# Optimization experiments

Hardware: AMD Instinct MI355X
Metric: run time of the kernel (lower is better)

Reference implementation:

```python
import jax, jax.numpy as jnp
import numpy as np

L, B, S, CACHE = 2, 1, 2048, 2048
H, HKV, D, DM, FF, V = 16, 8, 128, 2048, 8192, 32000
EPS = 1e-6
ROPE_BASE = 10000.0


def setup_inputs() -> dict:
    key = jax.random.key(0)
    ks = jax.random.split(key, 18)
    std = 0.02
    r = lambda k, shape: (jax.random.normal(k, shape, dtype=jnp.float32) * std)
    return {
        "input_ids": jax.random.randint(ks[0], (B, S), 0, V),
        "embed": r(ks[1], (V, DM)),
        "Wq": r(ks[2], (L, DM, H * D)),
        "Wk": r(ks[3], (L, DM, HKV * D)),
        "Wv": r(ks[4], (L, DM, HKV * D)),
        "Wo": r(ks[5], (L, H * D, DM)),
        "Wg": r(ks[6], (L, DM, FF)),
        "Wu": r(ks[7], (L, DM, FF)),
        "Wd": r(ks[8], (L, FF, DM)),
        "ln1": jnp.ones((L, DM), jnp.float32),
        "ln2": jnp.ones((L, DM), jnp.float32),
        "final_norm": jnp.ones((DM,), jnp.float32),
        "lm_head": r(ks[9], (DM, V)),
        "k_cache": jax.random.normal(ks[10], (L, B, H, CACHE, D), jnp.float32),
        "v_cache": jax.random.normal(ks[11], (L, B, H, CACHE, D), jnp.float32),
    }


def rms_norm(x, w):
    return x * jax.lax.rsqrt(jnp.mean(x * x, axis=-1, keepdims=True) + EPS) * w


def apply_rope(x, pos):
    # x: [B,H,T,D], pos: [T]
    inv_freq = 1.0 / (ROPE_BASE ** (jnp.arange(0, D, 2, dtype=jnp.float32) / D))
    f = pos[:, None].astype(jnp.float32) * inv_freq[None, :]  # [T, D/2]
    emb = jnp.concatenate([f, f], axis=-1)                    # [T, D]
    cos, sin = jnp.cos(emb), jnp.sin(emb)
    rot = jnp.concatenate([-x[..., D // 2:], x[..., : D // 2]], axis=-1)
    return x * cos + rot * sin


def decoder_forward(input_ids, embed, Wq, Wk, Wv, Wo, Wg, Wu, Wd,
                    ln1, ln2, final_norm, lm_head, k_cache, v_cache):
    h = embed[input_ids]  # [B,S,DM]
    T = CACHE + S
    q_pos = jnp.arange(CACHE, CACHE + S)
    k_pos = jnp.arange(T)
    # causal mask: query i (global pos CACHE+i) attends keys <= CACHE+i
    mask = k_pos[None, :] <= (CACHE + jnp.arange(S))[:, None]  # [S,T]
    scale = 1.0 / np.sqrt(D)

    def layer(h, params):
        wq, wk, wv, wo, wg, wu, wd, l1, l2, kc, vc = params
        x = rms_norm(h, l1)
        q = (x @ wq).reshape(B, S, H, D).transpose(0, 2, 1, 3)     # [B,H,S,D]
        k = (x @ wk).reshape(B, S, HKV, D).transpose(0, 2, 1, 3)   # [B,HKV,S,D]
        v = (x @ wv).reshape(B, S, HKV, D).transpose(0, 2, 1, 3)
        k = jnp.repeat(k, H // HKV, axis=1)                        # repeat_kv
        v = jnp.repeat(v, H // HKV, axis=1)
        k = jnp.concatenate([kc, k], axis=2)                       # [B,H,T,D]
        v = jnp.concatenate([vc, v], axis=2)
        q = apply_rope(q, q_pos)
        k = apply_rope(k, k_pos)
        scores = jnp.einsum('bhqd,bhkd->bhqk', q, k) * scale
        scores = jnp.where(mask, scores, jnp.float32(-1e30))
        attn = jax.nn.softmax(scores, axis=-1)
        o = jnp.einsum('bhqk,bhkd->bhqd', attn, v)
        o = o.transpose(0, 2, 1, 3).reshape(B, S, H * D) @ wo
        h = h + o
        x = rms_norm(h, l2)
        h = h + (jax.nn.silu(x @ wg) * (x @ wu)) @ wd
        return h, None

    h, _ = jax.lax.scan(layer, h, (Wq, Wk, Wv, Wo, Wg, Wu, Wd, ln1, ln2, k_cache, v_cache))
    h = rms_norm(h, final_norm)
    return (h @ lm_head).astype(jnp.float32)  # logits [B,S,V]


def reference(input_ids, embed, Wq, Wk, Wv, Wo, Wg, Wu, Wd,
              ln1, ln2, final_norm, lm_head, k_cache, v_cache):
    return decoder_forward(input_ids, embed, Wq, Wk, Wv, Wo, Wg, Wu, Wd,
                           ln1, ln2, final_norm, lm_head, k_cache, v_cache)
```

## Files before the change

### kernel.cpp

```cpp
#include <hip/hip_runtime.h>

typedef __attribute__((ext_vector_type(8))) short bfrag8;
typedef __attribute__((ext_vector_type(4))) short bfrag4;
typedef __attribute__((ext_vector_type(4))) float facc4;

#define DEV_INLINE __device__ __forceinline__

DEV_INLINE short f2bf(float f) {
    union { float f; unsigned u; } x; x.f = f;
    unsigned r = (x.u + 0x7FFFu + ((x.u >> 16) & 1u)) >> 16;
    return (short)r;
}

DEV_INLINE float bf2f(short s) {
    union { unsigned u; float f; } x;
    x.u = ((unsigned)(unsigned short)s) << 16;
    return x.f;
}

DEV_INLINE unsigned pack_bf2(float a, float b) {
    return (unsigned)(unsigned short)f2bf(a) | ((unsigned)(unsigned short)f2bf(b) << 16);
}

#define GL2LDS(gp, lp) __builtin_amdgcn_global_load_lds( \
    (const __attribute__((address_space(1))) void*)(gp), \
    (__attribute__((address_space(3))) void*)(lp), 16, 0, 0)

#define MFMA16(a, b, c) __builtin_amdgcn_mfma_f32_16x16x32_bf16((a), (b), (c), 0, 0, 0)

__global__ __launch_bounds__(256) void embed_kernel(const int* __restrict__ ids,
                                                    const float* __restrict__ emb,
                                                    float* __restrict__ h) {
    int s = blockIdx.x;
    int id = ids[s];
    const float* src = emb + (size_t)id * 2048;
    float* dst = h + (size_t)s * 2048;
    int t = threadIdx.x;
    float4 a = *(const float4*)(src + t * 8);
    float4 b = *(const float4*)(src + t * 8 + 4);
    *(float4*)(dst + t * 8) = a;
    *(float4*)(dst + t * 8 + 4) = b;
}

__global__ __launch_bounds__(256) void rmsnorm_bf16_kernel(const float* __restrict__ in,
                                                           const float* __restrict__ w,
                                                           short* __restrict__ out) {
    int row = blockIdx.x;
    const float* x = in + (size_t)row * 2048;
    short* y = out + (size_t)row * 2048;
    int t = threadIdx.x;
    float4 a = *(const float4*)(x + t * 8);
    float4 b = *(const float4*)(x + t * 8 + 4);
    float ss = a.x*a.x + a.y*a.y + a.z*a.z + a.w*a.w
             + b.x*b.x + b.y*b.y + b.z*b.z + b.w*b.w;
#pragma unroll
    for (int off = 32; off >= 1; off >>= 1) ss += __shfl_xor(ss, off);
    __shared__ float red[4];
    if ((t & 63) == 0) red[t >> 6] = ss;
    __syncthreads();
    float tot = red[0] + red[1] + red[2] + red[3];
    float sc = rsqrtf(tot * (1.0f / 2048.0f) + 1e-6f);
    float4 wa = *(const float4*)(w + t * 8);
    float4 wb = *(const float4*)(w + t * 8 + 4);
    bfrag8 o;
    o[0] = f2bf(a.x * sc * wa.x); o[1] = f2bf(a.y * sc * wa.y);
    o[2] = f2bf(a.z * sc * wa.z); o[3] = f2bf(a.w * sc * wa.w);
    o[4] = f2bf(b.x * sc * wb.x); o[5] = f2bf(b.y * sc * wb.y);
    o[6] = f2bf(b.z * sc * wb.z); o[7] = f2bf(b.w * sc * wb.w);
    *(bfrag8*)(y + t * 8) = o;
}

__global__ __launch_bounds__(256) void wconv_kernel(const float* __restrict__ W,
                                                    short* __restrict__ Wt,
                                                    int K, int N) {
    __shared__ short Lt[64][72];
    int k0 = blockIdx.x * 64, n0 = blockIdx.y * 64;
    int tid = threadIdx.x;
    int r = tid >> 4, c = (tid & 15) * 4;
#pragma unroll
    for (int j = 0; j < 4; ++j) {
        int k = r + j * 16;
        float4 v = *(const float4*)(W + (size_t)(k0 + k) * N + n0 + c);
        Lt[c + 0][k] = f2bf(v.x); Lt[c + 1][k] = f2bf(v.y);
        Lt[c + 2][k] = f2bf(v.z); Lt[c + 3][k] = f2bf(v.w);
    }
    __syncthreads();
    int n = tid >> 3, kk = (tid & 7) * 8;
#pragma unroll
    for (int j = 0; j < 2; ++j)
        *(bfrag8*)(Wt + (size_t)(n0 + n + j * 32) * K + k0 + kk) = *(const bfrag8*)&Lt[n + j * 32][kk];
}

template<int OUT>
__global__ __launch_bounds__(256, 2) void gemmR(const short* __restrict__ A,
                                                const short* __restrict__ Bt,
                                                float* __restrict__ C,
                                                int K, int N) {
    constexpr int ASLOT = 128 * 64;
    constexpr int BOFF = 4 * ASLOT;
    __shared__ short lds[4 * 256 * 32];
    char* ldsb = (char*)lds;
    int tid = threadIdx.x;
    int lane = tid & 63, wave = tid >> 6;
    int wm = wave >> 1, wn = wave & 1;
    int lr = lane & 15, lg = lane >> 4;

    int gx = gridDim.x;
    int nwg = gx * gridDim.y;
    int b = blockIdx.y * gx + blockIdx.x;
    int q8 = nwg >> 3, r8 = nwg & 7;
    int xcd = b & 7, idx = b >> 3;
    int lb = (xcd < r8) ? (xcd * (q8 + 1) + idx) : (r8 * (q8 + 1) + (xcd - r8) * q8 + idx);
    int bm = (lb % gx) * 128, bn = (lb / gx) * 128;

    facc4 acc[4][4];
#pragma unroll
    for (int m = 0; m < 4; ++m)
#pragma unroll
        for (int n = 0; n < 4; ++n) acc[m][n] = (facc4){0.f, 0.f, 0.f, 0.f};

    int rs = tid >> 2;
    int cs = (tid & 3) ^ ((rs >> 1) & 3);
    const size_t sK = (size_t)K;
    const short* Ag0 = A + (size_t)(bm + rs) * sK + cs * 8;
    const short* Ag1 = A + (size_t)(bm + rs + 64) * sK + cs * 8;
    const short* Bg0 = Bt + (size_t)(bn + rs) * sK + cs * 8;
    const short* Bg1 = Bt + (size_t)(bn + rs + 64) * sK + cs * 8;

    auto stage = [&](int u) {
        int sl = u & 3;
        int ko = u * 32;
        char* Ad = ldsb + sl * ASLOT + tid * 16;
        char* Bd = ldsb + BOFF + sl * ASLOT + tid * 16;
        GL2LDS(Ag0 + ko, Ad);
        GL2LDS(Ag1 + ko, Ad + 4096);
        GL2LDS(Bg0 + ko, Bd);
        GL2LDS(Bg1 + ko, Bd + 4096);
    };

    int NT = K >> 5;
    stage(0); stage(1); stage(2);

    int arow[4], brow[4];
#pragma unroll
    for (int m = 0; m < 4; ++m) arow[m] = wm * 64 + m * 16 + lr;
#pragma unroll
    for (int n = 0; n < 4; ++n) brow[n] = wn * 64 + n * 16 + lr;

    for (int t = 0; t < NT; ++t) {
        if (t < NT - 2)       asm volatile("s_waitcnt vmcnt(8)" ::: "memory");
        else if (t == NT - 2) asm volatile("s_waitcnt vmcnt(4)" ::: "memory");
        else                  asm volatile("s_waitcnt vmcnt(0)" ::: "memory");
        __builtin_amdgcn_s_barrier();
        __builtin_amdgcn_sched_barrier(0);
        const char* Ab = ldsb + (t & 3) * ASLOT;
        const char* Bb = ldsb + BOFF + (t & 3) * ASLOT;
        bfrag8 af[4], bf[4];
#pragma unroll
        for (int m = 0; m < 4; ++m) {
            int r = arow[m];
            af[m] = *(const bfrag8*)(Ab + r * 64 + ((lg ^ ((r >> 1) & 3)) << 4));
        }
#pragma unroll
        for (int n = 0; n < 4; ++n) {
            int r = brow[n];
            bf[n] = *(const bfrag8*)(Bb + r * 64 + ((lg ^ ((r >> 1) & 3)) << 4));
        }
        if (t + 3 < NT) stage(t + 3);
        __builtin_amdgcn_s_setprio(1);
#pragma unroll
        for (int m = 0; m < 4; ++m)
#pragma unroll
            for (int n = 0; n < 4; ++n)
                acc[m][n] = MFMA16(af[m], bf[n], acc[m][n]);
        __builtin_amdgcn_s_setprio(0);
    }

    int crow = bm + wm * 64 + lg * 4;
    int ccol = bn + wn * 64 + lr;
#pragma unroll
    for (int m = 0; m < 4; ++m)
#pragma unroll
        for (int n = 0; n < 4; ++n)
#pragma unroll
            for (int r = 0; r < 4; ++r) {
                size_t ci = (size_t)(crow + m * 16 + r) * N + ccol + n * 16;
                if constexpr (OUT == 0)      C[ci] = acc[m][n][r];
                else if constexpr (OUT == 1) C[ci] = C[ci] + acc[m][n][r];
                else                         ((short*)C)[ci] = f2bf(acc[m][n][r]);
            }
}

template<int OUT>
__global__ __launch_bounds__(512, 2) void gemm8p(const short* __restrict__ A,
                                                 const short* __restrict__ Bt,
                                                 float* __restrict__ C,
                                                 int K, int N) {
    __shared__ short lds[49152];
    char* ldsb = (char*)lds;
    int tid = threadIdx.x;
    int lane = tid & 63, wave = tid >> 6;
    int wm = wave >> 2, wn = wave & 3;
    int lr = lane & 15, lg = lane >> 4;

    int gx = gridDim.x;
    int nwg = gx * gridDim.y;
    int b = blockIdx.y * gx + blockIdx.x;
    int q8 = nwg >> 3, r8 = nwg & 7;
    int xcd = b & 7, idx = b >> 3;
    int lb = (xcd < r8) ? (xcd * (q8 + 1) + idx) : (r8 * (q8 + 1) + (xcd - r8) * q8 + idx);
    int bm = (lb % gx) * 256, bn = (lb / gx) * 256;

    facc4 acc[8][4];
#pragma unroll
    for (int m = 0; m < 8; ++m)
#pragma unroll
        for (int n = 0; n < 4; ++n) acc[m][n] = (facc4){0.f, 0.f, 0.f, 0.f};

    int rs = tid >> 2;
    int cs = (tid & 3) ^ ((rs >> 1) & 3);
    const size_t sK = (size_t)K;
    const short* Agl = A + (size_t)(bm + rs) * sK + cs * 8;
    const short* Agh = A + (size_t)(bm + rs + 128) * sK + cs * 8;
    const short* Bgl = Bt + (size_t)(bn + rs) * sK + cs * 8;
    const short* Bgh = Bt + (size_t)(bn + rs + 128) * sK + cs * 8;

    auto stage = [&](int h) {
        int sb = (h % 3) * 16384;
        int ko = h * 32;
        GL2LDS(Agl + ko, ldsb + sb + tid * 16);
        GL2LDS(Agh + ko, ldsb + sb + 8192 + tid * 16);
        GL2LDS(Bgl + ko, ldsb + 49152 + sb + tid * 16);
        GL2LDS(Bgh + ko, ldsb + 49152 + sb + 8192 + tid * 16);
    };

    int H = K >> 5;
    stage(0); stage(1);

    int arow[8], brow[4];
#pragma unroll
    for (int m = 0; m < 8; ++m) arow[m] = wm * 128 + m * 16 + lr;
#pragma unroll
    for (int n = 0; n < 4; ++n) brow[n] = wn * 64 + n * 16 + lr;

    for (int h = 0; h < H; ++h) {
        if (h + 1 < H) asm volatile("s_waitcnt vmcnt(4)" ::: "memory");
        else           asm volatile("s_waitcnt vmcnt(0)" ::: "memory");
        __builtin_amdgcn_s_barrier();
        __builtin_amdgcn_sched_barrier(0);
        const char* Ah = ldsb + (h % 3) * 16384;
        const char* Bh = ldsb + 49152 + (h % 3) * 16384;
        bfrag8 af[8], bf[4];
#pragma unroll
        for (int m = 0; m < 8; ++m) {
            int r = arow[m];
            af[m] = *(const bfrag8*)(Ah + r * 64 + ((lg ^ ((r >> 1) & 3)) << 4));
        }
#pragma unroll
        for (int n = 0; n < 2; ++n) {
            int r = brow[n];
            bf[n] = *(const bfrag8*)(Bh + r * 64 + ((lg ^ ((r >> 1) & 3)) << 4));
        }
        if (h + 2 < H) stage(h + 2);
        __builtin_amdgcn_s_barrier();
        asm volatile("s_waitcnt lgkmcnt(0)" ::: "memory");
        __builtin_amdgcn_sched_barrier(0);
        __builtin_amdgcn_s_setprio(1);
#pragma unroll
        for (int m = 0; m < 8; ++m) {
            acc[m][0] = MFMA16(af[m], bf[0], acc[m][0]);
            acc[m][1] = MFMA16(af[m], bf[1], acc[m][1]);
        }
        __builtin_amdgcn_s_setprio(0);
        __builtin_amdgcn_s_barrier();
#pragma unroll
        for (int n = 2; n < 4; ++n) {
            int r = brow[n];
            bf[n] = *(const bfrag8*)(Bh + r * 64 + ((lg ^ ((r >> 1) & 3)) << 4));
        }
        __builtin_amdgcn_s_barrier();
        asm volatile("s_waitcnt lgkmcnt(0)" ::: "memory");
        __builtin_amdgcn_sched_barrier(0);
        __builtin_amdgcn_s_setprio(1);
#pragma unroll
        for (int m = 0; m < 8; ++m) {
            acc[m][2] = MFMA16(af[m], bf[2], acc[m][2]);
            acc[m][3] = MFMA16(af[m], bf[3], acc[m][3]);
        }
        __builtin_amdgcn_s_setprio(0);
    }

    int crow = bm + wm * 128 + lg * 4;
    int ccol = bn + wn * 64 + lr;
#pragma unroll
    for (int m = 0; m < 8; ++m)
#pragma unroll
        for (int n = 0; n < 4; ++n)
#pragma unroll
            for (int r = 0; r < 4; ++r) {
                size_t ci = (size_t)(crow + m * 16 + r) * N + ccol + n * 16;
                if constexpr (OUT == 0)      C[ci] = acc[m][n][r];
                else if constexpr (OUT == 1) C[ci] = C[ci] + acc[m][n][r];
                else                         ((short*)C)[ci] = f2bf(acc[m][n][r]);
            }
}

#define ROPE_C 0.20762050593046010f
#define INV2PI 0.15915494309189535f
#define TWOPI  6.283185307179586f
#define QK_SCALE 0.08838834764831845f

DEV_INLINE void rope_sc(float pos, int j, float* s, float* c) {
    float f = pos * exp2f(-(float)j * ROPE_C);
    float r = f * INV2PI;
    r -= floorf(r);
    __sincosf(r * TWOPI, s, c);
}

__global__ __launch_bounds__(128) void prep_q_kernel(const float* __restrict__ qkv,
                                                     short* __restrict__ Qb) {
    int h = blockIdx.x, s = blockIdx.y, d = threadIdx.x;
    const float* src = qkv + (size_t)s * 4096 + h * 128;
    float x = src[d], xp = src[d ^ 64];
    float sn, c;
    rope_sc((float)(2048 + s), d & 63, &sn, &c);
    float o = (d < 64) ? (x * c - xp * sn) : (x * c + xp * sn);
    Qb[((size_t)h * 2048 + s) * 128 + d] = f2bf(o * QK_SCALE);
}

__global__ __launch_bounds__(128) void prep_k_kernel(const float* __restrict__ kc,
                                                     const float* __restrict__ qkv,
                                                     short* __restrict__ Kf) {
    int h = blockIdx.x, t = blockIdx.y, d = threadIdx.x;
    float x, xp;
    if (t < 2048) {
        const float* src = kc + ((size_t)h * 2048 + t) * 128;
        x = src[d]; xp = src[d ^ 64];
    } else {
        const float* src = qkv + (size_t)(t - 2048) * 4096 + 2048 + (h >> 1) * 128;
        x = src[d]; xp = src[d ^ 64];
    }
    float sn, c;
    rope_sc((float)t, d & 63, &sn, &c);
    float o = (d < 64) ? (x * c - xp * sn) : (x * c + xp * sn);
    Kf[((size_t)h * 4096 + t) * 128 + d] = f2bf(o);
}

__global__ __launch_bounds__(256) void prep_v_kernel(const float* __restrict__ vc,
                                                     const float* __restrict__ qkv,
                                                     short* __restrict__ Vt) {
    int h = blockIdx.x;
    int t0 = blockIdx.y * 64;
    __shared__ short Lt[128][72];
    int tid = threadIdx.x;
    int r = tid >> 2;
    int c0 = (tid & 3) * 32;
    int t = t0 + r;
    const float* src = (t < 2048)
        ? vc + ((size_t)h * 2048 + t) * 128 + c0
        : qkv + (size_t)(t - 2048) * 4096 + 3072 + (h >> 1) * 128 + c0;
#pragma unroll
    for (int i = 0; i < 32; i += 4) {
        float4 v = *(const float4*)(src + i);
        Lt[c0 + i + 0][r] = f2bf(v.x);
        Lt[c0 + i + 1][r] = f2bf(v.y);
        Lt[c0 + i + 2][r] = f2bf(v.z);
        Lt[c0 + i + 3][r] = f2bf(v.w);
    }
    __syncthreads();
    int d = tid >> 1;
    int hh = (tid & 1) * 32;
    short* dst = Vt + ((size_t)h * 128 + d) * 4096 + t0 + hh;
    const short* srcl = &Lt[d][hh];
#pragma unroll
    for (int i = 0; i < 32; i += 8)
        *(bfrag8*)(dst + i) = *(const bfrag8*)(srcl + i);
}

__global__ __launch_bounds__(256, 4) void attn_kernel(const short* __restrict__ Q,
                                                      const short* __restrict__ Kf,
                                                      const short* __restrict__ Vt,
                                                      float* __restrict__ Op,
                                                      float* __restrict__ Ml,
                                                      float* __restrict__ Ll) {
    int h = blockIdx.x;
    int qb = blockIdx.y * 64;
    int z = blockIdx.z;
    int tid = threadIdx.x;
    int lane = tid & 63, wave = tid >> 6;
    int lr = lane & 15, lg = lane >> 4;
    int qrow = qb + wave * 16;
    int qg = 2048 + qrow + lr;

    __shared__ short Ks[2][4096];
    __shared__ short Vs[2][4096];
    __shared__ short P[4][16][40];

    const short* kbase = Kf + (size_t)h * 4096 * 128;
    const short* vbase = Vt + (size_t)h * 128 * 4096;

    bfrag8 aq[4];
    {
        const short* qp = Q + ((size_t)h * 2048 + qrow + lr) * 128 + lg * 8;
#pragma unroll
        for (int dt = 0; dt < 4; ++dt) aq[dt] = *(const bfrag8*)(qp + dt * 32);
    }
    facc4 o[8];
#pragma unroll
    for (int n = 0; n < 8; ++n) o[n] = (facc4){0.f, 0.f, 0.f, 0.f};
    float m = -1e30f, l = 0.f;

    auto stage = [&](int buf, int t0) {
#pragma unroll
        for (int half = 0; half < 2; ++half) {
            int rk = half * 16 + wave * 4 + (lane >> 4);
            int ck = (lane & 15) ^ (rk & 7);
            GL2LDS(kbase + (size_t)(t0 + rk) * 128 + ck * 8,
                   &Ks[buf][half * 2048 + wave * 512 + lane * 8]);
            int rv = half * 64 + wave * 16 + (lane >> 2);
            int cv = (lane & 3) ^ ((rv >> 1) & 3);
            GL2LDS(vbase + (size_t)rv * 4096 + t0 + cv * 8,
                   &Vs[buf][half * 2048 + wave * 512 + lane * 8]);
        }
    };

    auto process = [&](int buf, int t0) {
        facc4 s0 = (facc4){0.f, 0.f, 0.f, 0.f}, s1 = (facc4){0.f, 0.f, 0.f, 0.f};
        int r0 = lr, r1 = 16 + lr;
#pragma unroll
        for (int dt = 0; dt < 4; ++dt) {
            bfrag8 k0 = *(const bfrag8*)&Ks[buf][r0 * 128 + (((dt * 4 + lg) ^ (r0 & 7)) * 8)];
            bfrag8 k1 = *(const bfrag8*)&Ks[buf][r1 * 128 + (((dt * 4 + lg) ^ (r1 & 7)) * 8)];
            s0 = MFMA16(k0, aq[dt], s0);
            s1 = MFMA16(k1, aq[dt], s1);
        }
        float mx = m;
#pragma unroll
        for (int r = 0; r < 4; ++r) {
            int k0i = t0 + lg * 4 + r;
            if (k0i > qg)      s0[r] = -1e30f;
            if (k0i + 16 > qg) s1[r] = -1e30f;
            mx = fmaxf(mx, fmaxf(s0[r], s1[r]));
        }
        mx = fmaxf(mx, __shfl_xor(mx, 16));
        mx = fmaxf(mx, __shfl_xor(mx, 32));
        if (__any(mx > m + 8.f)) {
            float alpha = __expf(m - mx);
            m = mx;
            l *= alpha;
            float ab[4];
#pragma unroll
            for (int r = 0; r < 4; ++r) ab[r] = __shfl(alpha, lg * 4 + r);
#pragma unroll
            for (int n = 0; n < 8; ++n) {
                o[n][0] *= ab[0]; o[n][1] *= ab[1]; o[n][2] *= ab[2]; o[n][3] *= ab[3];
            }
        }
        float ps = 0.f;
#pragma unroll
        for (int r = 0; r < 4; ++r) {
            s0[r] = __expf(s0[r] - m); ps += s0[r];
            s1[r] = __expf(s1[r] - m); ps += s1[r];
        }
        ps += __shfl_xor(ps, 16);
        ps += __shfl_xor(ps, 32);
        l += ps;
        unsigned* prow = (unsigned*)&P[wave][lr][0];
        prow[lg * 2]     = pack_bf2(s0[0], s0[1]);
        prow[lg * 2 + 1] = pack_bf2(s0[2], s0[3]);
        prow[8 + lg * 2]     = pack_bf2(s1[0], s1[1]);
        prow[8 + lg * 2 + 1] = pack_bf2(s1[2], s1[3]);
        bfrag8 ap = *(const bfrag8*)&P[wave][lr][lg * 8];
#pragma unroll
        for (int n = 0; n < 8; ++n) {
            int rv = n * 16 + lr;
            bfrag8 vf = *(const bfrag8*)&Vs[buf][rv * 32 + ((lg ^ ((rv >> 1) & 3)) * 8)];
            o[n] = MFMA16(ap, vf, o[n]);
        }
    };

    int NT = ((2048 + qb + 63) >> 5) + 1;
    int i0 = z ? (NT >> 1) : 0;
    int i1 = z ? NT : (NT >> 1);

    stage(0, i0 * 32);
    __syncthreads();
    int buf = 0;
    for (int i = i0; i < i1; ++i) {
        if (i + 1 < i1) stage(buf ^ 1, (i + 1) * 32);
        process(buf, i * 32);
        __syncthreads();
        buf ^= 1;
    }

#pragma unroll
    for (int n = 0; n < 8; ++n)
#pragma unroll
        for (int r = 0; r < 4; ++r)
            Op[(size_t)(z * 2048 + qrow + lg * 4 + r) * 2048 + h * 128 + n * 16 + lr] = o[n][r];
    if (lg == 0) {
        Ml[((size_t)z * 16 + h) * 2048 + qrow + lr] = m;
        Ll[((size_t)z * 16 + h) * 2048 + qrow + lr] = l;
    }
}

__global__ __launch_bounds__(256) void attn_combine(const float* __restrict__ Op,
                                                    const float* __restrict__ Ml,
                                                    const float* __restrict__ Ll,
                                                    short* __restrict__ Ob) {
    int row = blockIdx.x, t = threadIdx.x;
    int col0 = t * 8;
    int h = col0 >> 7;
    float m0 = Ml[(size_t)h * 2048 + row], m1 = Ml[(size_t)(16 + h) * 2048 + row];
    float l0 = Ll[(size_t)h * 2048 + row], l1 = Ll[(size_t)(16 + h) * 2048 + row];
    float mm = fmaxf(m0, m1);
    float a0 = __expf(m0 - mm), a1 = __expf(m1 - mm);
    float inv = 1.f / (l0 * a0 + l1 * a1);
    a0 *= inv; a1 *= inv;
    const float* p0 = Op + (size_t)row * 2048 + col0;
    const float* p1 = Op + (size_t)(2048 + row) * 2048 + col0;
    float4 x0 = *(const float4*)p0, x1 = *(const float4*)(p0 + 4);
    float4 y0 = *(const float4*)p1, y1 = *(const float4*)(p1 + 4);
    bfrag8 ov;
    ov[0] = f2bf(x0.x * a0 + y0.x * a1); ov[1] = f2bf(x0.y * a0 + y0.y * a1);
    ov[2] = f2bf(x0.z * a0 + y0.z * a1); ov[3] = f2bf(x0.w * a0 + y0.w * a1);
    ov[4] = f2bf(x1.x * a0 + y1.x * a1); ov[5] = f2bf(x1.y * a0 + y1.y * a1);
    ov[6] = f2bf(x1.z * a0 + y1.z * a1); ov[7] = f2bf(x1.w * a0 + y1.w * a1);
    *(bfrag8*)(Ob + (size_t)row * 2048 + col0) = ov;
}

__global__ __launch_bounds__(256) void silu_fused_kernel(const short* __restrict__ f,
                                                         short* __restrict__ out) {
    size_t v = (size_t)blockIdx.x * 256 + threadIdx.x;
    int r = (int)(v >> 10);
    int c = (int)(v & 1023) * 8;
    bfrag8 g = *(const bfrag8*)(f + (size_t)r * 16384 + c);
    bfrag8 u = *(const bfrag8*)(f + (size_t)r * 16384 + 8192 + c);
    bfrag8 o;
#pragma unroll
    for (int j = 0; j < 8; ++j) {
        float gf = bf2f(g[j]), uf = bf2f(u[j]);
        o[j] = f2bf(gf / (1.f + __expf(-gf)) * uf);
    }
    *(bfrag8*)(out + v * 8) = o;
}

extern "C" void kernel_launch(void* const* d_in, const int* in_sizes, int n_in,
                              void* d_out, int out_size, void* d_ws, size_t ws_size,
                              hipStream_t stream) {
    const int*   ids   = (const int*)d_in[0];
    const float* emb   = (const float*)d_in[1];
    const float* Wq    = (const float*)d_in[2];
    const float* Wk    = (const float*)d_in[3];
    const float* Wv    = (const float*)d_in[4];
    const float* Wo    = (const float*)d_in[5];
    const float* Wg    = (const float*)d_in[6];
    const float* Wu    = (const float*)d_in[7];
    const float* Wd    = (const float*)d_in[8];
    const float* ln1   = (const float*)d_in[9];
    const float* ln2   = (const float*)d_in[10];
    const float* fnorm = (const float*)d_in[11];
    const float* lmh   = (const float*)d_in[12];
    const float* kc    = (const float*)d_in[13];
    const float* vc    = (const float*)d_in[14];
    float* logits = (float*)d_out;

    char* ws = (char*)d_ws;
    float* hbuf   = (float*)(ws + ((size_t)0 << 20));
    short* xb     = (short*)(ws + ((size_t)16 << 20));
    float* qkvbuf = (float*)(ws + ((size_t)24 << 20));
    short* Ob     = (short*)(ws + ((size_t)56 << 20));
    short* wt     = (short*)(ws + ((size_t)64 << 20));
    short* Qb     = (short*)(ws + ((size_t)128 << 20));
    short* Kf     = (short*)(ws + ((size_t)136 << 20));
    short* Vt     = (short*)(ws + ((size_t)152 << 20));
    short* fbuf   = (short*)(ws + ((size_t)168 << 20));
    short* gb     = (short*)(ws + ((size_t)232 << 20));
    float* mlb    = (float*)(ws + ((size_t)264 << 20));
    float* Mlp    = mlb;
    float* Llp    = mlb + 2 * 16 * 2048;
    short* lmwt   = (short*)(ws + ((size_t)64 << 20));

    embed_kernel<<<2048, 256, 0, stream>>>(ids, emb, hbuf);

    for (int l = 0; l < 2; ++l) {
        const float* wq  = Wq + (size_t)l * 2048 * 2048;
        const float* wk  = Wk + (size_t)l * 2048 * 1024;
        const float* wv  = Wv + (size_t)l * 2048 * 1024;
        const float* wo  = Wo + (size_t)l * 2048 * 2048;
        const float* wg  = Wg + (size_t)l * 2048 * 8192;
        const float* wu  = Wu + (size_t)l * 2048 * 8192;
        const float* wd  = Wd + (size_t)l * 8192 * 2048;
        const float* l1  = ln1 + (size_t)l * 2048;
        const float* l2  = ln2 + (size_t)l * 2048;
        const float* kcl = kc + (size_t)l * 16 * 2048 * 128;
        const float* vcl = vc + (size_t)l * 16 * 2048 * 128;

        rmsnorm_bf16_kernel<<<2048, 256, 0, stream>>>(hbuf, l1, xb);
        wconv_kernel<<<dim3(32, 32), 256, 0, stream>>>(wq, wt, 2048, 2048);
        wconv_kernel<<<dim3(32, 16), 256, 0, stream>>>(wk, wt + (size_t)2048 * 2048, 2048, 1024);
        wconv_kernel<<<dim3(32, 16), 256, 0, stream>>>(wv, wt + (size_t)3072 * 2048, 2048, 1024);
        gemmR<0><<<dim3(16, 32), 256, 0, stream>>>(xb, wt, qkvbuf, 2048, 4096);
        prep_q_kernel<<<dim3(16, 2048), 128, 0, stream>>>(qkvbuf, Qb);
        prep_k_kernel<<<dim3(16, 4096), 128, 0, stream>>>(kcl, qkvbuf, Kf);
        prep_v_kernel<<<dim3(16, 64), 256, 0, stream>>>(vcl, qkvbuf, Vt);
        attn_kernel<<<dim3(16, 32, 2), 256, 0, stream>>>(Qb, Kf, Vt, qkvbuf, Mlp, Llp);
        attn_combine<<<2048, 256, 0, stream>>>(qkvbuf, Mlp, Llp, Ob);
        wconv_kernel<<<dim3(32, 32), 256, 0, stream>>>(wo, wt, 2048, 2048);
        gemmR<1><<<dim3(16, 16), 256, 0, stream>>>(Ob, wt, hbuf, 2048, 2048);
        rmsnorm_bf16_kernel<<<2048, 256, 0, stream>>>(hbuf, l2, xb);
        wconv_kernel<<<dim3(32, 128), 256, 0, stream>>>(wg, wt, 2048, 8192);
        wconv_kernel<<<dim3(32, 128), 256, 0, stream>>>(wu, wt + (size_t)8192 * 2048, 2048, 8192);
        gemm8p<2><<<dim3(8, 64), 512, 0, stream>>>(xb, wt, (float*)fbuf, 2048, 16384);
        silu_fused_kernel<<<8192, 256, 0, stream>>>(fbuf, gb);
        wconv_kernel<<<dim3(128, 32), 256, 0, stream>>>(wd, wt, 8192, 2048);
        gemmR<1><<<dim3(16, 16), 256, 0, stream>>>(gb, wt, hbuf, 8192, 2048);
    }
    rmsnorm_bf16_kernel<<<2048, 256, 0, stream>>>(hbuf, fnorm, xb);
    wconv_kernel<<<dim3(32, 500), 256, 0, stream>>>(lmh, lmwt, 2048, 32000);
    gemm8p<0><<<dim3(8, 125), 512, 0, stream>>>(xb, lmwt, logits, 2048, 32000);
}
```

Before: 1.569 ms.

## Replace ping-pong 256x256 GEMM with 4-stage pipeline and double attention KV tile

Replaces the gemm8p kernel, which used a 3-slot LDS ring and split-phase barriers, with gemmB. gemmB uses a 4-slot LDS ring (128KB), stages three tiles ahead, loads all fragments in one pass and runs 1 block per CU. Separately, the attention kernel now processes 64 keys per iteration instead of 32, with larger K/V/P LDS buffers and occupancy lowered to 2. The goal is to hide more memory latency and cut loop and barrier overhead per tile, at the cost of lower occupancy and more LDS pressure.

Result: no change. 1.550 ms (-1.2%).

```diff
diff --git a/kernel.cpp b/kernel.cpp
--- a/kernel.cpp
+++ b/kernel.cpp
@@ -92,6 +92,106 @@
 }
 
 template<int OUT>
+__global__ __launch_bounds__(512, 1) void gemmB(const short* __restrict__ A,
+                                                const short* __restrict__ Bt,
+                                                float* __restrict__ C,
+                                                int K, int N) {
+    constexpr int ASLOT = 256 * 64;
+    constexpr int BOFF = 4 * ASLOT;
+    __shared__ short lds[65536];
+    char* ldsb = (char*)lds;
+    int tid = threadIdx.x;
+    int lane = tid & 63, wave = tid >> 6;
+    int wm = wave >> 2, wn = wave & 3;
+    int lr = lane & 15, lg = lane >> 4;
+
+    int gx = gridDim.x;
+    int nwg = gx * gridDim.y;
+    int b = blockIdx.y * gx + blockIdx.x;
+    int q8 = nwg >> 3, r8 = nwg & 7;
+    int xcd = b & 7, idx = b >> 3;
+    int lb = (xcd < r8) ? (xcd * (q8 + 1) + idx) : (r8 * (q8 + 1) + (xcd - r8) * q8 + idx);
+    int bm = (lb % gx) * 256, bn = (lb / gx) * 256;
+
+    facc4 acc[8][4];
+#pragma unroll
+    for (int m = 0; m < 8; ++m)
+#pragma unroll
+        for (int n = 0; n < 4; ++n) acc[m][n] = (facc4){0.f, 0.f, 0.f, 0.f};
+
+    int rs = tid >> 2;
+    int cs = (tid & 3) ^ ((rs >> 1) & 3);
+    const size_t sK = (size_t)K;
+    const short* Ag0 = A + (size_t)(bm + rs) * sK + cs * 8;
+    const short* Ag1 = A + (size_t)(bm + rs + 128) * sK + cs * 8;
+    const short* Bg0 = Bt + (size_t)(bn + rs) * sK + cs * 8;
+    const short* Bg1 = Bt + (size_t)(bn + rs + 128) * sK + cs * 8;
+
+    auto stage = [&](int u) {
+        int sl = u & 3;
+        int ko = u * 32;
+        char* Ad = ldsb + sl * ASLOT + tid * 16;
+        char* Bd = ldsb + BOFF + sl * ASLOT + tid * 16;
+        GL2LDS(Ag0 + ko, Ad);
+        GL2LDS(Ag1 + ko, Ad + 8192);
+        GL2LDS(Bg0 + ko, Bd);
+        GL2LDS(Bg1 + ko, Bd + 8192);
+    };
+
+    int NT = K >> 5;
+    stage(0); stage(1); stage(2);
+
+    int arow[8], brow[4];
+#pragma unroll
+    for (int m = 0; m < 8; ++m) arow[m] = wm * 128 + m * 16 + lr;
+#pragma unroll
+    for (int n = 0; n < 4; ++n) brow[n] = wn * 64 + n * 16 + lr;
+
+    for (int t = 0; t < NT; ++t) {
+        if (t < NT - 2)       asm volatile("s_waitcnt vmcnt(8)" ::: "memory");
+        else if (t == NT - 2) asm volatile("s_waitcnt vmcnt(4)" ::: "memory");
+        else                  asm volatile("s_waitcnt vmcnt(0)" ::: "memory");
+        __builtin_amdgcn_s_barrier();
+        __builtin_amdgcn_sched_barrier(0);
+        const char* Ab = ldsb + (t & 3) * ASLOT;
+        const char* Bb = ldsb + BOFF + (t & 3) * ASLOT;
+        bfrag8 af[8], bf[4];
+#pragma unroll
+        for (int m = 0; m < 8; ++m) {
+            int r = arow[m];
+            af[m] = *(const bfrag8*)(Ab + r * 64 + ((lg ^ ((r >> 1) & 3)) << 4));
+        }
+#pragma unroll
+        for (int n = 0; n < 4; ++n) {
+            int r = brow[n];
+            bf[n] = *(const bfrag8*)(Bb + r * 64 + ((lg ^ ((r >> 1) & 3)) << 4));
+        }
+        if (t + 3 < NT) stage(t + 3);
+        __builtin_amdgcn_s_setprio(1);
+#pragma unroll
+        for (int m = 0; m < 8; ++m)
+#pragma unroll
+            for (int n = 0; n < 4; ++n)
+                acc[m][n] = MFMA16(af[m], bf[n], acc[m][n]);
+        __builtin_amdgcn_s_setprio(0);
+    }
+
+    int crow = bm + wm * 128 + lg * 4;
+    int ccol = bn + wn * 64 + lr;
+#pragma unroll
+    for (int m = 0; m < 8; ++m)
+#pragma unroll
+        for (int n = 0; n < 4; ++n)
+#pragma unroll
+            for (int r = 0; r < 4; ++r) {
+                size_t ci = (size_t)(crow + m * 16 + r) * N + ccol + n * 16;
+                if constexpr (OUT == 0)      C[ci] = acc[m][n][r];
+                else if constexpr (OUT == 1) C[ci] = C[ci] + acc[m][n][r];
+                else                         ((short*)C)[ci] = f2bf(acc[m][n][r]);
+            }
+}
+
+template<int OUT>
 __global__ __launch_bounds__(256, 2) void gemmR(const short* __restrict__ A,
                                                 const short* __restrict__ Bt,
                                                 float* __restrict__ C,
@@ -180,120 +280,6 @@
     int ccol = bn + wn * 64 + lr;
 #pragma unroll
     for (int m = 0; m < 4; ++m)
-#pragma unroll
-        for (int n = 0; n < 4; ++n)
-#pragma unroll
-            for (int r = 0; r < 4; ++r) {
-                size_t ci = (size_t)(crow + m * 16 + r) * N + ccol + n * 16;
-                if constexpr (OUT == 0)      C[ci] = acc[m][n][r];
-                else if constexpr (OUT == 1) C[ci] = C[ci] + acc[m][n][r];
-                else                         ((short*)C)[ci] = f2bf(acc[m][n][r]);
-            }
-}
-
-template<int OUT>
-__global__ __launch_bounds__(512, 2) void gemm8p(const short* __restrict__ A,
-                                                 const short* __restrict__ Bt,
-                                                 float* __restrict__ C,
-                                                 int K, int N) {
-    __shared__ short lds[49152];
-    char* ldsb = (char*)lds;
-    int tid = threadIdx.x;
-    int lane = tid & 63, wave = tid >> 6;
-    int wm = wave >> 2, wn = wave & 3;
-    int lr = lane & 15, lg = lane >> 4;
-
-    int gx = gridDim.x;
-    int nwg = gx * gridDim.y;
-    int b = blockIdx.y * gx + blockIdx.x;
-    int q8 = nwg >> 3, r8 = nwg & 7;
-    int xcd = b & 7, idx = b >> 3;
-    int lb = (xcd < r8) ? (xcd * (q8 + 1) + idx) : (r8 * (q8 + 1) + (xcd - r8) * q8 + idx);
-    int bm = (lb % gx) * 256, bn = (lb / gx) * 256;
-
-    facc4 acc[8][4];
-#pragma unroll
-    for (int m = 0; m < 8; ++m)
-#pragma unroll
-        for (int n = 0; n < 4; ++n) acc[m][n] = (facc4){0.f, 0.f, 0.f, 0.f};
-
-    int rs = tid >> 2;
-    int cs = (tid & 3) ^ ((rs >> 1) & 3);
-    const size_t sK = (size_t)K;
-    const short* Agl = A + (size_t)(bm + rs) * sK + cs * 8;
-    const short* Agh = A + (size_t)(bm + rs + 128) * sK + cs * 8;
-    const short* Bgl = Bt + (size_t)(bn + rs) * sK + cs * 8;
-    const short* Bgh = Bt + (size_t)(bn + rs + 128) * sK + cs * 8;
-
-    auto stage = [&](int h) {
-        int sb = (h % 3) * 16384;
-        int ko = h * 32;
-        GL2LDS(Agl + ko, ldsb + sb + tid * 16);
-        GL2LDS(Agh + ko, ldsb + sb + 8192 + tid * 16);
-        GL2LDS(Bgl + ko, ldsb + 49152 + sb + tid * 16);
-        GL2LDS(Bgh + ko, ldsb + 49152 + sb + 8192 + tid * 16);
-    };
-
-    int H = K >> 5;
-    stage(0); stage(1);
-
-    int arow[8], brow[4];
-#pragma unroll
-    for (int m = 0; m < 8; ++m) arow[m] = wm * 128 + m * 16 + lr;
-#pragma unroll
-    for (int n = 0; n < 4; ++n) brow[n] = wn * 64 + n * 16 + lr;
-
-    for (int h = 0; h < H; ++h) {
-        if (h + 1 < H) asm volatile("s_waitcnt vmcnt(4)" ::: "memory");
-        else           asm volatile("s_waitcnt vmcnt(0)" ::: "memory");
-        __builtin_amdgcn_s_barrier();
-        __builtin_amdgcn_sched_barrier(0);
-        const char* Ah = ldsb + (h % 3) * 16384;
-        const char* Bh = ldsb + 49152 + (h % 3) * 16384;
-        bfrag8 af[8], bf[4];
-#pragma unroll
-        for (int m = 0; m < 8; ++m) {
-            int r = arow[m];
-            af[m] = *(const bfrag8*)(Ah + r * 64 + ((lg ^ ((r >> 1) & 3)) << 4));
-        }
-#pragma unroll
-        for (int n = 0; n < 2; ++n) {
-            int r = brow[n];
-            bf[n] = *(const bfrag8*)(Bh + r * 64 + ((lg ^ ((r >> 1) & 3)) << 4));
-        }
-        if (h + 2 < H) stage(h + 2);
-        __builtin_amdgcn_s_barrier();
-        asm volatile("s_waitcnt lgkmcnt(0)" ::: "memory");
-        __builtin_amdgcn_sched_barrier(0);
-        __builtin_amdgcn_s_setprio(1);
-#pragma unroll
-        for (int m = 0; m < 8; ++m) {
-            acc[m][0] = MFMA16(af[m], bf[0], acc[m][0]);
-            acc[m][1] = MFMA16(af[m], bf[1], acc[m][1]);
-        }
-        __builtin_amdgcn_s_setprio(0);
-        __builtin_amdgcn_s_barrier();
-#pragma unroll
-        for (int n = 2; n < 4; ++n) {
-            int r = brow[n];
-            bf[n] = *(const bfrag8*)(Bh + r * 64 + ((lg ^ ((r >> 1) & 3)) << 4));
-        }
-        __builtin_amdgcn_s_barrier();
-        asm volatile("s_waitcnt lgkmcnt(0)" ::: "memory");
-        __builtin_amdgcn_sched_barrier(0);
-        __builtin_amdgcn_s_setprio(1);
-#pragma unroll
-        for (int m = 0; m < 8; ++m) {
-            acc[m][2] = MFMA16(af[m], bf[2], acc[m][2]);
-            acc[m][3] = MFMA16(af[m], bf[3], acc[m][3]);
-        }
-        __builtin_amdgcn_s_setprio(0);
-    }
-
-    int crow = bm + wm * 128 + lg * 4;
-    int ccol = bn + wn * 64 + lr;
-#pragma unroll
-    for (int m = 0; m < 8; ++m)
 #pragma unroll
         for (int n = 0; n < 4; ++n)
 #pragma unroll
@@ -377,7 +363,7 @@
         *(bfrag8*)(dst + i) = *(const bfrag8*)(srcl + i);
 }
 
-__global__ __launch_bounds__(256, 4) void attn_kernel(const short* __restrict__ Q,
+__global__ __launch_bounds__(256, 2) void attn_kernel(const short* __restrict__ Q,
                                                       const short* __restrict__ Kf,
                                                       const short* __restrict__ Vt,
                                                       float* __restrict__ Op,
@@ -392,9 +378,9 @@
     int qrow = qb + wave * 16;
     int qg = 2048 + qrow + lr;
 
-    __shared__ short Ks[2][4096];
-    __shared__ short Vs[2][4096];
-    __shared__ short P[4][16][40];
+    __shared__ short Ks[2][8192];
+    __shared__ short Vs[2][8192];
+    __shared__ short P[4][16][72];
 
     const short* kbase = Kf + (size_t)h * 4096 * 128;
     const short* vbase = Vt + (size_t)h * 128 * 4096;
@@ -412,36 +398,39 @@
 
     auto stage = [&](int buf, int t0) {
 #pragma unroll
-        for (int half = 0; half < 2; ++half) {
-            int rk = half * 16 + wave * 4 + (lane >> 4);
-            int ck = (lane & 15) ^ (rk & 7);
+        for (int it = 0; it < 4; ++it) {
+            int rk = it * 16 + (tid >> 4);
+            int ck = (tid & 15) ^ (rk & 7);
             GL2LDS(kbase + (size_t)(t0 + rk) * 128 + ck * 8,
-                   &Ks[buf][half * 2048 + wave * 512 + lane * 8]);
-            int rv = half * 64 + wave * 16 + (lane >> 2);
-            int cv = (lane & 3) ^ ((rv >> 1) & 3);
+                   &Ks[buf][it * 2048 + tid * 8]);
+            int rv = it * 32 + (tid >> 3);
+            int cv = (tid & 7) ^ (rv & 7);
             GL2LDS(vbase + (size_t)rv * 4096 + t0 + cv * 8,
-                   &Vs[buf][half * 2048 + wave * 512 + lane * 8]);
+                   &Vs[buf][it * 2048 + tid * 8]);
         }
     };
 
     auto process = [&](int buf, int t0) {
-        facc4 s0 = (facc4){0.f, 0.f, 0.f, 0.f}, s1 = (facc4){0.f, 0.f, 0.f, 0.f};
-        int r0 = lr, r1 = 16 + lr;
-#pragma unroll
-        for (int dt = 0; dt < 4; ++dt) {
-            bfrag8 k0 = *(const bfrag8*)&Ks[buf][r0 * 128 + (((dt * 4 + lg) ^ (r0 & 7)) * 8)];
-            bfrag8 k1 = *(const bfrag8*)&Ks[buf][r1 * 128 + (((dt * 4 + lg) ^ (r1 & 7)) * 8)];
-            s0 = MFMA16(k0, aq[dt], s0);
-            s1 = MFMA16(k1, aq[dt], s1);
+        facc4 s[4];
+#pragma unroll
+        for (int j = 0; j < 4; ++j) {
+            s[j] = (facc4){0.f, 0.f, 0.f, 0.f};
+            int r = j * 16 + lr;
+#pragma unroll
+            for (int dt = 0; dt < 4; ++dt) {
+                bfrag8 k = *(const bfrag8*)&Ks[buf][r * 128 + (((dt * 4 + lg) ^ (r & 7)) * 8)];
+                s[j] = MFMA16(k, aq[dt], s[j]);
+            }
         }
         float mx = m;
 #pragma unroll
-        for (int r = 0; r < 4; ++r) {
-            int k0i = t0 + lg * 4 + r;
-            if (k0i > qg)      s0[r] = -1e30f;
-            if (k0i + 16 > qg) s1[r] = -1e30f;
-            mx = fmaxf(mx, fmaxf(s0[r], s1[r]));
-        }
+        for (int j = 0; j < 4; ++j)
+#pragma unroll
+            for (int r = 0; r < 4; ++r) {
+                int ki = t0 + j * 16 + lg * 4 + r;
+                if (ki > qg) s[j][r] = -1e30f;
+                mx = fmaxf(mx, s[j][r]);
+            }
         mx = fmaxf(mx, __shfl_xor(mx, 16));
         mx = fmaxf(mx, __shfl_xor(mx, 32));
         if (__any(mx > m + 8.f)) {
@@ -458,37 +447,43 @@
         }
         float ps = 0.f;
 #pragma unroll
-        for (int r = 0; r < 4; ++r) {
-            s0[r] = __expf(s0[r] - m); ps += s0[r];
-            s1[r] = __expf(s1[r] - m); ps += s1[r];
-        }
+        for (int j = 0; j < 4; ++j)
+#pragma unroll
+            for (int r = 0; r < 4; ++r) {
+                s[j][r] = __expf(s[j][r] - m);
+                ps += s[j][r];
+            }
         ps += __shfl_xor(ps, 16);
         ps += __shfl_xor(ps, 32);
         l += ps;
         unsigned* prow = (unsigned*)&P[wave][lr][0];
-        prow[lg * 2]     = pack_bf2(s0[0], s0[1]);
-        prow[lg * 2 + 1] = pack_bf2(s0[2], s0[3]);
-        prow[8 + lg * 2]     = pack_bf2(s1[0], s1[1]);
-        prow[8 + lg * 2 + 1] = pack_bf2(s1[2], s1[3]);
-        bfrag8 ap = *(const bfrag8*)&P[wave][lr][lg * 8];
+#pragma unroll
+        for (int j = 0; j < 4; ++j) {
+            prow[j * 8 + lg * 2]     = pack_bf2(s[j][0], s[j][1]);
+            prow[j * 8 + lg * 2 + 1] = pack_bf2(s[j][2], s[j][3]);
+        }
+        bfrag8 ap0 = *(const bfrag8*)&P[wave][lr][lg * 8];
+        bfrag8 ap1 = *(const bfrag8*)&P[wave][lr][32 + lg * 8];
 #pragma unroll
         for (int n = 0; n < 8; ++n) {
             int rv = n * 16 + lr;
-            bfrag8 vf = *(const bfrag8*)&Vs[buf][rv * 32 + ((lg ^ ((rv >> 1) & 3)) * 8)];
-            o[n] = MFMA16(ap, vf, o[n]);
+            bfrag8 v0 = *(const bfrag8*)&Vs[buf][rv * 64 + (((lg) ^ (rv & 7)) * 8)];
+            bfrag8 v1 = *(const bfrag8*)&Vs[buf][rv * 64 + (((4 + lg) ^ (rv & 7)) * 8)];
+            o[n] = MFMA16(ap0, v0, o[n]);
+            o[n] = MFMA16(ap1, v1, o[n]);
         }
     };
 
-    int NT = ((2048 + qb + 63) >> 5) + 1;
+    int NT = (2048 + qb + 64) >> 6;
     int i0 = z ? (NT >> 1) : 0;
     int i1 = z ? NT : (NT >> 1);
 
-    stage(0, i0 * 32);
+    stage(0, i0 * 64);
     __syncthreads();
     int buf = 0;
     for (int i = i0; i < i1; ++i) {
-        if (i + 1 < i1) stage(buf ^ 1, (i + 1) * 32);
-        process(buf, i * 32);
+        if (i + 1 < i1) stage(buf ^ 1, (i + 1) * 64);
+        process(buf, i * 64);
         __syncthreads();
         buf ^= 1;
     }
@@ -611,12 +606,12 @@
         rmsnorm_bf16_kernel<<<2048, 256, 0, stream>>>(hbuf, l2, xb);
         wconv_kernel<<<dim3(32, 128), 256, 0, stream>>>(wg, wt, 2048, 8192);
         wconv_kernel<<<dim3(32, 128), 256, 0, stream>>>(wu, wt + (size_t)8192 * 2048, 2048, 8192);
-        gemm8p<2><<<dim3(8, 64), 512, 0, stream>>>(xb, wt, (float*)fbuf, 2048, 16384);
+        gemmB<2><<<dim3(8, 64), 512, 0, stream>>>(xb, wt, (float*)fbuf, 2048, 16384);
         silu_fused_kernel<<<8192, 256, 0, stream>>>(fbuf, gb);
         wconv_kernel<<<dim3(128, 32), 256, 0, stream>>>(wd, wt, 8192, 2048);
         gemmR<1><<<dim3(16, 16), 256, 0, stream>>>(gb, wt, hbuf, 8192, 2048);
     }
     rmsnorm_bf16_kernel<<<2048, 256, 0, stream>>>(hbuf, fnorm, xb);
     wconv_kernel<<<dim3(32, 500), 256, 0, stream>>>(lmh, lmwt, 2048, 32000);
-    gemm8p<0><<<dim3(8, 125), 512, 0, stream>>>(xb, lmwt, logits, 2048, 32000);
-}
+    gemmB<0><<<dim3(8, 125), 512, 0, stream>>>(xb, lmwt, logits, 2048, 32000);
+}
```
